# Performance work log

Hardware: AMD Instinct MI355X
Metric: run time of the kernel (lower is better)

Reference implementation:

```python
import jax, jax.numpy as jnp
import numpy as np

B, S, E, H, Dh = 2, 2048, 1024, 16, 64


def setup_inputs() -> dict:
    key = jax.random.key(0)
    ks = jax.random.split(key, 12)
    scale = 1.0 / np.sqrt(E)
    inp = {
        "query": jax.random.normal(ks[0], (B, S, E), jnp.float32),
        "key_": jax.random.normal(ks[1], (B, S, E), jnp.float32),
        "value": jax.random.normal(ks[2], (B, S, E), jnp.float32),
        # causal mask, broadcast over heads inside reference (mask==0 -> -inf)
        "mask": jnp.broadcast_to(jnp.tril(jnp.ones((S, S), jnp.int32)), (B, S, S)),
        "WQ": jax.random.normal(ks[3], (E, H * Dh), jnp.float32) * scale,
        "bQ": jnp.zeros((H * Dh,), jnp.float32),
        "WK": jax.random.normal(ks[4], (E, H * Dh), jnp.float32) * scale,
        "bK": jnp.zeros((H * Dh,), jnp.float32),
        "WV": jax.random.normal(ks[5], (E, H * Dh), jnp.float32) * scale,
        "bV": jnp.zeros((H * Dh,), jnp.float32),
        "WO": jax.random.normal(ks[6], (H * Dh, E), jnp.float32) * scale,
        "bO": jnp.zeros((E,), jnp.float32),
    }
    return inp


def reference(query, key_, value, mask, WQ, bQ, WK, bK, WV, bV, WO, bO):
    # projections -> [B, H, S, Dh]
    def proj(x, W, b):
        y = x @ W + b  # [B, S, H*Dh]
        return y.reshape(B, -1, H, Dh).transpose(0, 2, 1, 3)

    q = proj(query, WQ, bQ)
    k = proj(key_, WK, bK)
    v = proj(value, WV, bV)

    # scores [B, H, S, S]
    a = jnp.einsum("bhqd,bhkd->bhqk", q, k) / jnp.sqrt(jnp.float32(Dh))
    a = jnp.where(mask[:, None, :, :] == 0, -jnp.inf, a)
    alpha = jax.nn.softmax(a, axis=-1)
    z = jnp.einsum("bhqk,bhkd->bhqd", alpha, v)  # [B, H, S, Dh]
    z = z.transpose(0, 2, 1, 3).reshape(B, -1, H * Dh)
    return z @ WO + bO
```

## Files before the change

### kernel.cpp

```cpp
#include <hip/hip_runtime.h>
#include <hip/hip_bf16.h>
#include <math.h>

namespace {

constexpr int Bb = 2, Ss = 2048, Ee = 1024, Hh = 16, Dh = 64;
constexpr int M  = Bb * Ss;
constexpr int N  = Hh * Dh;
constexpr int Kd = Ee;

typedef __attribute__((ext_vector_type(8))) short bf16x8;
typedef __attribute__((ext_vector_type(4))) float f32x4;

__device__ inline unsigned short f2bf(float f) {
  return __builtin_bit_cast(unsigned short, __float2bfloat16(f));
}
__device__ inline unsigned pack2(float a, float b) {
  return (unsigned)f2bf(a) | ((unsigned)f2bf(b) << 16);
}
__device__ inline void load_lds16(const void* g, void* lds) {
  __builtin_amdgcn_global_load_lds((const __attribute__((address_space(1))) void*)g,
                                   (__attribute__((address_space(3))) void*)lds, 16, 0, 0);
}

__global__ __launch_bounds__(256) void convert3(const float* __restrict__ a0,
                                                const float* __restrict__ a1,
                                                const float* __restrict__ a2,
                                                unsigned short* __restrict__ o0,
                                                unsigned short* __restrict__ o1,
                                                unsigned short* __restrict__ o2) {
  const float* src = blockIdx.z == 0 ? a0 : (blockIdx.z == 1 ? a1 : a2);
  unsigned short* dst = blockIdx.z == 0 ? o0 : (blockIdx.z == 1 ? o1 : o2);
  size_t i = ((size_t)blockIdx.x * 256 + threadIdx.x) * 8;
  float4 u = ((const float4*)(src + i))[0];
  float4 v = ((const float4*)(src + i))[1];
  uint4 w;
  w.x = pack2(u.x, u.y);
  w.y = pack2(u.z, u.w);
  w.z = pack2(v.x, v.y);
  w.w = pack2(v.z, v.w);
  *((uint4*)(dst + i)) = w;
}

__global__ __launch_bounds__(256) void transposeW(const float* __restrict__ w0,
                                                  const float* __restrict__ w1,
                                                  const float* __restrict__ w2,
                                                  const float* __restrict__ w3,
                                                  unsigned short* __restrict__ t0,
                                                  unsigned short* __restrict__ t1,
                                                  unsigned short* __restrict__ t2,
                                                  unsigned short* __restrict__ t3) {
  const float* W = blockIdx.z == 0 ? w0 : (blockIdx.z == 1 ? w1 : (blockIdx.z == 2 ? w2 : w3));
  unsigned short* Wt = blockIdx.z == 0 ? t0 : (blockIdx.z == 1 ? t1 : (blockIdx.z == 2 ? t2 : t3));
  __shared__ float tl[32][33];
  const int t = threadIdx.x;
  const int r = t >> 5, c = t & 31;
  const int n0 = blockIdx.x * 32, k0 = blockIdx.y * 32;
#pragma unroll
  for (int i = 0; i < 4; ++i) tl[r + i * 8][c] = W[(size_t)(k0 + r + i * 8) * N + n0 + c];
  __syncthreads();
#pragma unroll
  for (int i = 0; i < 4; ++i) {
    int rr = r + i * 8;
    Wt[(size_t)(n0 + rr) * Kd + k0 + c] = f2bf(tl[c][rr]);
  }
}

__device__ __attribute__((always_inline)) inline void gemm_core(
    const unsigned short* __restrict__ A, const unsigned short* __restrict__ Wt,
    unsigned short* As0, unsigned short* As1, unsigned short* Bs0,
    unsigned short* Bs1, f32x4 (&acc)[4][4]) {
  const int t = threadIdx.x, l = t & 63, w = t >> 6;
  const int wr = w >> 1, wc = w & 1, lr = l & 15, kc = l >> 4;
  const int bm = blockIdx.y * 128, bn = blockIdx.x * 128;
  const int srow = t >> 2, sc4 = t & 3;
  const unsigned short* Ap1 = A + (size_t)(bm + srow) * Kd + sc4 * 8;
  const unsigned short* Ap2 = Ap1 + (size_t)64 * Kd;
  const unsigned short* Bp1 = Wt + (size_t)(bn + srow) * Kd + sc4 * 8;
  const unsigned short* Bp2 = Bp1 + (size_t)64 * Kd;
  const size_t d1 = (size_t)(w * 64) * 8, d2 = (size_t)(w * 64 + 256) * 8;

  auto stage = [&](unsigned short* Ab, unsigned short* Bb, int kk) {
    load_lds16(Ap1 + kk, Ab + d1);
    load_lds16(Ap2 + kk, Ab + d2);
    load_lds16(Bp1 + kk, Bb + d1);
    load_lds16(Bp2 + kk, Bb + d2);
  };
  auto compute = [&](const unsigned short* Ab, const unsigned short* Bb) {
    bf16x8 a[4], b[4];
#pragma unroll
    for (int m = 0; m < 4; ++m)
      a[m] = *(const bf16x8*)&Ab[(size_t)(wr * 64 + m * 16 + lr) * 32 + kc * 8];
#pragma unroll
    for (int n = 0; n < 4; ++n)
      b[n] = *(const bf16x8*)&Bb[(size_t)(wc * 64 + n * 16 + lr) * 32 + kc * 8];
#pragma unroll
    for (int m = 0; m < 4; ++m)
#pragma unroll
      for (int n = 0; n < 4; ++n)
        acc[m][n] = __builtin_amdgcn_mfma_f32_16x16x32_bf16(a[m], b[n], acc[m][n], 0, 0, 0);
  };

  stage(As0, Bs0, 0);
  __syncthreads();
  for (int kk = 0; kk < Kd; kk += 64) {
    if (kk + 32 < Kd) stage(As1, Bs1, kk + 32);
    compute(As0, Bs0);
    __syncthreads();
    if (kk + 64 < Kd) stage(As0, Bs0, kk + 64);
    compute(As1, Bs1);
    __syncthreads();
  }
}

__global__ __launch_bounds__(256) void qkv_gemm(
    const unsigned short* __restrict__ qb, const unsigned short* __restrict__ kb,
    const unsigned short* __restrict__ vb, const unsigned short* __restrict__ wqT,
    const unsigned short* __restrict__ wkT, const unsigned short* __restrict__ wvT,
    const float* __restrict__ bQ, const float* __restrict__ bK,
    const float* __restrict__ bV, unsigned short* __restrict__ Qw,
    unsigned short* __restrict__ Kw, unsigned short* __restrict__ Vt) {
  __shared__ alignas(16) unsigned short smem[4][128 * 32];
  const int z = blockIdx.z;
  const unsigned short* A  = z == 0 ? qb : (z == 1 ? kb : vb);
  const unsigned short* Wt = z == 0 ? wqT : (z == 1 ? wkT : wvT);
  const float* bias        = z == 0 ? bQ : (z == 1 ? bK : bV);

  f32x4 acc[4][4] = {};
  gemm_core(A, Wt, smem[0], smem[1], smem[2], smem[3], acc);

  const int t = threadIdx.x, l = t & 63, w = t >> 6;
  const int wr = w >> 1, wc = w & 1, lr = l & 15, kc = l >> 4;
  const int bm = blockIdx.y * 128, bn = blockIdx.x * 128;

  if (z <= 1) {
    unsigned short* Cout = z ? Kw : Qw;
    const float oscale = z ? 1.0f : 0.125f;
#pragma unroll
    for (int m = 0; m < 4; ++m)
#pragma unroll
      for (int n = 0; n < 4; ++n) {
        const int cg = bn + wc * 64 + n * 16 + lr;
        const float bv = bias[cg];
#pragma unroll
        for (int r = 0; r < 4; ++r) {
          const int rg = bm + wr * 64 + m * 16 + kc * 4 + r;
          const int b_ = rg >> 11, s = rg & (Ss - 1);
          const int h = cg >> 6, d = cg & 63;
          Cout[(((size_t)(b_ * Hh + h) * Ss + s) << 6) + d] =
              f2bf((acc[m][n][r] + bv) * oscale);
        }
      }
  } else {
    unsigned short(*Ct)[136] = reinterpret_cast<unsigned short(*)[136]>(&smem[0][0]);
    const int b_ = bm >> 11, sb = bm & (Ss - 1);
#pragma unroll
    for (int nh = 0; nh < 2; ++nh) {
      if (wc == nh) {
#pragma unroll
        for (int m = 0; m < 4; ++m)
#pragma unroll
          for (int n = 0; n < 4; ++n) {
            const int cg = bn + wc * 64 + n * 16 + lr;
            const float bv = bias[cg];
            const int cl = n * 16 + lr;
            const int s0 = wr * 64 + m * 16 + kc * 4;
            ushort4 pk;
            pk.x = f2bf(acc[m][n][0] + bv);
            pk.y = f2bf(acc[m][n][1] + bv);
            pk.z = f2bf(acc[m][n][2] + bv);
            pk.w = f2bf(acc[m][n][3] + bv);
            *(ushort4*)&Ct[cl][s0] = pk;
          }
      }
      __syncthreads();
#pragma unroll
      for (int i = 0; i < 4; ++i) {
        const int c = i * 256 + t;
        const int cl = c >> 4, ch = c & 15;
        const int cg = bn + nh * 64 + cl;
        const int h = cg >> 6, d = cg & 63;
        uint4 vv = *(const uint4*)&Ct[cl][ch * 8];
        *(uint4*)(Vt + (((size_t)(b_ * Hh + h) * Dh + d) << 11) + sb + ch * 8) = vv;
      }
      __syncthreads();
    }
  }
}

__global__ __launch_bounds__(256) void gemm_out(const unsigned short* __restrict__ A,
                                                const unsigned short* __restrict__ Wt,
                                                const float* __restrict__ bias,
                                                float* __restrict__ C) {
  __shared__ alignas(16) unsigned short smem[4][128 * 32];
  f32x4 acc[4][4] = {};
  gemm_core(A, Wt, smem[0], smem[1], smem[2], smem[3], acc);

  const int t = threadIdx.x, l = t & 63, w = t >> 6;
  const int wr = w >> 1, wc = w & 1, lr = l & 15, kc = l >> 4;
  const int bm = blockIdx.y * 128, bn = blockIdx.x * 128;
#pragma unroll
  for (int m = 0; m < 4; ++m)
#pragma unroll
    for (int n = 0; n < 4; ++n) {
      const int cg = bn + wc * 64 + n * 16 + lr;
      const float bv = bias[cg];
#pragma unroll
      for (int r = 0; r < 4; ++r) {
        const int rg = bm + wr * 64 + m * 16 + kc * 4 + r;
        C[(size_t)rg * N + cg] = acc[m][n][r] + bv;
      }
    }
}

__global__ __launch_bounds__(256) void attn_mfma(const unsigned short* __restrict__ Q,
                                                 const unsigned short* __restrict__ K,
                                                 const unsigned short* __restrict__ Vt,
                                                 unsigned short* __restrict__ Z) {
  __shared__ alignas(16) unsigned short Ks[64 * 64];
  __shared__ alignas(16) unsigned short Vs[64 * 64];
  __shared__ alignas(16) unsigned short Ps[4][16 * 64];

  const int bh  = blockIdx.x;
  const int qtA = blockIdx.y;
  const int qtB = (Ss / 64 - 1) - qtA;
  const int b  = bh >> 4, h = bh & 15;
  const int t  = threadIdx.x;
  const int l  = t & 63;
  const int w  = t >> 6;
  const int lr = l & 15;
  const int lg = l >> 4;

  const int qrowA = qtA * 64 + w * 16 + lr;
  const int qrowB = qtB * 64 + w * 16 + lr;
  const unsigned short* QpA = Q + ((size_t)bh * Ss + qrowA) * Dh;
  const unsigned short* QpB = Q + ((size_t)bh * Ss + qrowB) * Dh;
  bf16x8 bqA[2], bqB[2];
  bqA[0] = *(const bf16x8*)(QpA + lg * 8);
  bqA[1] = *(const bf16x8*)(QpA + 32 + lg * 8);
  bqB[0] = *(const bf16x8*)(QpB + lg * 8);
  bqB[1] = *(const bf16x8*)(QpB + 32 + lg * 8);

  f32x4 oA[4] = {}, oB[4] = {};
  float mA = -INFINITY, lA = 0.f, mB = -INFINITY, lB = 0.f;

  const int srow = l >> 3;
  const int scol = ((l & 7) ^ srow) * 16;
  const char* Kg = (const char*)(K + (size_t)bh * Ss * Dh);
  const char* Vg = (const char*)(Vt + (size_t)bh * Dh * Ss);
  unsigned short* kD0 = Ks + (w * 16) * 64;
  unsigned short* kD1 = Ks + (w * 16 + 8) * 64;
  unsigned short* vD0 = Vs + (w * 16) * 64;
  unsigned short* vD1 = Vs + (w * 16 + 8) * 64;
  const char* vr0 = Vg + (size_t)(w * 16 + srow) * (Ss * 2) + scol;
  const char* vr1 = Vg + (size_t)(w * 16 + 8 + srow) * (Ss * 2) + scol;

  const int rx = (lr & 7) << 4;

  auto process = [&](const bf16x8 (&bq)[2], f32x4 (&o)[4], float& mrow,
                     float& lsum, int qrow, bool diag, int kv0) {
    f32x4 sa[4];
    __builtin_amdgcn_s_setprio(1);
#pragma unroll
    for (int f = 0; f < 4; ++f) {
      sa[f] = (f32x4){0.f, 0.f, 0.f, 0.f};
#pragma unroll
      for (int kk = 0; kk < 2; ++kk) {
        const int cb = (kk * 64 + lg * 16) ^ rx;
        bf16x8 ak = *(const bf16x8*)((const char*)Ks + (f * 16 + lr) * 128 + cb);
        sa[f] = __builtin_amdgcn_mfma_f32_16x16x32_bf16(ak, bq[kk], sa[f], 0, 0, 0);
      }
    }
    __builtin_amdgcn_s_setprio(0);

    if (diag) {
#pragma unroll
      for (int f = 0; f < 4; ++f)
#pragma unroll
        for (int r = 0; r < 4; ++r) {
          const int kg = kv0 + f * 16 + lg * 4 + r;
          if (kg > qrow) sa[f][r] = -INFINITY;
        }
    }

    float pmax = sa[0][0];
#pragma unroll
    for (int f = 0; f < 4; ++f)
#pragma unroll
      for (int r = 0; r < 4; ++r) pmax = fmaxf(pmax, sa[f][r]);
    pmax = fmaxf(pmax, __shfl_xor(pmax, 16));
    pmax = fmaxf(pmax, __shfl_xor(pmax, 32));

    if (!__all(pmax <= mrow + 8.f)) {
      const float mnew = fmaxf(mrow, pmax);
      const float sc = __expf(mrow - mnew);
      lsum *= sc;
      float scr[4];
#pragma unroll
      for (int r = 0; r < 4; ++r) scr[r] = __shfl(sc, lg * 4 + r);
#pragma unroll
      for (int n = 0; n < 4; ++n)
#pragma unroll
        for (int r = 0; r < 4; ++r) o[n][r] *= scr[r];
      mrow = mnew;
    }

    float p[4][4];
    float psum = 0.f;
#pragma unroll
    for (int f = 0; f < 4; ++f)
#pragma unroll
      for (int r = 0; r < 4; ++r) {
        p[f][r] = __expf(sa[f][r] - mrow);
        psum += p[f][r];
      }
    psum += __shfl_xor(psum, 16);
    psum += __shfl_xor(psum, 32);
    lsum += psum;

    {
      char* Pw = (char*)Ps[w] + lr * 128;
#pragma unroll
      for (int f = 0; f < 4; ++f) {
        const int k0b = f * 32 + lg * 8;
        *(unsigned*)(Pw + ((k0b) ^ rx))     = pack2(p[f][0], p[f][1]);
        *(unsigned*)(Pw + ((k0b + 4) ^ rx)) = pack2(p[f][2], p[f][3]);
      }
    }

    __builtin_amdgcn_s_setprio(1);
#pragma unroll
    for (int kk = 0; kk < 2; ++kk) {
      const int cb = (kk * 64 + lg * 16) ^ rx;
      bf16x8 ap = *(const bf16x8*)((const char*)Ps[w] + lr * 128 + cb);
#pragma unroll
      for (int n = 0; n < 4; ++n) {
        bf16x8 bv = *(const bf16x8*)((const char*)Vs + (n * 16 + lr) * 128 + cb);
        o[n] = __builtin_amdgcn_mfma_f32_16x16x32_bf16(ap, bv, o[n], 0, 0, 0);
      }
    }
    __builtin_amdgcn_s_setprio(0);
  };

  for (int kt = 0; kt <= qtB; ++kt) {
    const int kv0 = kt * 64;
    __syncthreads();
    load_lds16(Kg + (size_t)(kv0 + w * 16 + srow) * 128 + scol, kD0);
    load_lds16(Kg + (size_t)(kv0 + w * 16 + 8 + srow) * 128 + scol, kD1);
    load_lds16(vr0 + kv0 * 2, vD0);
    load_lds16(vr1 + kv0 * 2, vD1);
    __syncthreads();

    process(bqB, oB, mB, lB, qrowB, kt == qtB, kv0);
    if (kt <= qtA) process(bqA, oA, mA, lA, qrowA, kt == qtA, kv0);
  }

  auto epilogue = [&](f32x4 (&o)[4], float lsum, int qt) {
    const float linv = 1.f / lsum;
    float li[4];
#pragma unroll
    for (int r = 0; r < 4; ++r) li[r] = __shfl(linv, lg * 4 + r);
#pragma unroll
    for (int n = 0; n < 4; ++n)
#pragma unroll
      for (int r = 0; r < 4; ++r) {
        const int qg = qt * 64 + w * 16 + lg * 4 + r;
        Z[((size_t)(b * Ss + qg)) * N + h * 64 + n * 16 + lr] =
            f2bf(o[n][r] * li[r]);
      }
  };
  epilogue(oA, lA, qtA);
  epilogue(oB, lB, qtB);
}

}

extern "C" void kernel_launch(void* const* d_in, const int* in_sizes, int n_in,
                              void* d_out, int out_size, void* d_ws, size_t ws_size,
                              hipStream_t stream) {
  const float* query = (const float*)d_in[0];
  const float* key_  = (const float*)d_in[1];
  const float* value = (const float*)d_in[2];
  const float* WQ = (const float*)d_in[4];
  const float* bQ = (const float*)d_in[5];
  const float* WK = (const float*)d_in[6];
  const float* bK = (const float*)d_in[7];
  const float* WV = (const float*)d_in[8];
  const float* bV = (const float*)d_in[9];
  const float* WO = (const float*)d_in[10];
  const float* bO = (const float*)d_in[11];
  float* out = (float*)d_out;

  const size_t mat = (size_t)M * N;
  unsigned short* qb  = (unsigned short*)d_ws;
  unsigned short* kb  = qb + mat;
  unsigned short* vb  = kb + mat;
  unsigned short* wqT = vb + mat;
  unsigned short* wkT = wqT + (size_t)N * Kd;
  unsigned short* wvT = wkT + (size_t)N * Kd;
  unsigned short* woT = wvT + (size_t)N * Kd;
  unsigned short* Qw  = woT + (size_t)N * Kd;
  unsigned short* Kw  = Qw + mat;
  unsigned short* Vw  = Kw + mat;
  unsigned short* zb  = qb;

  convert3<<<dim3(mat / 2048, 1, 3), 256, 0, stream>>>(query, key_, value, qb, kb, vb);
  transposeW<<<dim3(N / 32, Kd / 32, 4), 256, 0, stream>>>(WQ, WK, WV, WO, wqT, wkT, wvT, woT);

  qkv_gemm<<<dim3(N / 128, M / 128, 3), 256, 0, stream>>>(qb, kb, vb, wqT, wkT, wvT,
                                                          bQ, bK, bV, Qw, Kw, Vw);

  attn_mfma<<<dim3(Bb * Hh, Ss / 128), 256, 0, stream>>>(Qw, Kw, Vw, zb);

  gemm_out<<<dim3(N / 128, M / 128), 256, 0, stream>>>(zb, woT, bO, out);
}
```

Baseline: 255.3 us.

## Double-buffer K/V tiles in attention and deepen GEMM prefetch with vmcnt waits

The attention kernel now keeps two K/V tiles in LDS and prefetches tile kt+2 while computing on tile kt. The GEMM core keeps two stages in flight and replaces __syncthreads with explicit s_waitcnt vmcnt(4)/vmcnt(0) plus raw barriers. The goal is to hide global-to-LDS load latency behind MFMA work instead of stalling on it each iteration. In exchange the attention kernel doubles its LDS use for K/V, which may lower occupancy. Correctness depends on the hand-counted vmcnt values matching the number of outstanding loads per stage.

```diff
diff --git a/kernel.cpp b/kernel.cpp
--- a/kernel.cpp
+++ b/kernel.cpp
@@ -21,6 +21,18 @@
 __device__ inline void load_lds16(const void* g, void* lds) {
   __builtin_amdgcn_global_load_lds((const __attribute__((address_space(1))) void*)g,
                                    (__attribute__((address_space(3))) void*)lds, 16, 0, 0);
+}
+__device__ inline void wait_vm4_barrier() {
+  asm volatile("s_waitcnt vmcnt(4)" ::: "memory");
+  __builtin_amdgcn_s_barrier();
+}
+__device__ inline void wait_vm0_barrier() {
+  asm volatile("s_waitcnt vmcnt(0)" ::: "memory");
+  __builtin_amdgcn_s_barrier();
+}
+__device__ inline void barrier_then_fence() {
+  __builtin_amdgcn_s_barrier();
+  __builtin_amdgcn_sched_barrier(0);
 }
 
 __global__ __launch_bounds__(256) void convert3(const float* __restrict__ a0,
@@ -101,15 +113,20 @@
         acc[m][n] = __builtin_amdgcn_mfma_f32_16x16x32_bf16(a[m], b[n], acc[m][n], 0, 0, 0);
   };
 
+  constexpr int NT = Kd / 32;
   stage(As0, Bs0, 0);
-  __syncthreads();
-  for (int kk = 0; kk < Kd; kk += 64) {
-    if (kk + 32 < Kd) stage(As1, Bs1, kk + 32);
-    compute(As0, Bs0);
-    __syncthreads();
-    if (kk + 64 < Kd) stage(As0, Bs0, kk + 64);
-    compute(As1, Bs1);
-    __syncthreads();
+  stage(As1, Bs1, 32);
+#pragma unroll 2
+  for (int i = 0; i < NT; ++i) {
+    if (i + 1 < NT) wait_vm4_barrier();
+    else            wait_vm0_barrier();
+    if (i & 1) compute(As1, Bs1);
+    else       compute(As0, Bs0);
+    barrier_then_fence();
+    if (i + 2 < NT) {
+      if (i & 1) stage(As1, Bs1, (i + 2) * 32);
+      else       stage(As0, Bs0, (i + 2) * 32);
+    }
   }
 }
 
@@ -217,8 +234,8 @@
                                                  const unsigned short* __restrict__ K,
                                                  const unsigned short* __restrict__ Vt,
                                                  unsigned short* __restrict__ Z) {
-  __shared__ alignas(16) unsigned short Ks[64 * 64];
-  __shared__ alignas(16) unsigned short Vs[64 * 64];
+  __shared__ alignas(16) unsigned short Ks[2 * 64 * 64];
+  __shared__ alignas(16) unsigned short Vs[2 * 64 * 64];
   __shared__ alignas(16) unsigned short Ps[4][16 * 64];
 
   const int bh  = blockIdx.x;
@@ -248,17 +265,24 @@
   const int scol = ((l & 7) ^ srow) * 16;
   const char* Kg = (const char*)(K + (size_t)bh * Ss * Dh);
   const char* Vg = (const char*)(Vt + (size_t)bh * Dh * Ss);
-  unsigned short* kD0 = Ks + (w * 16) * 64;
-  unsigned short* kD1 = Ks + (w * 16 + 8) * 64;
-  unsigned short* vD0 = Vs + (w * 16) * 64;
-  unsigned short* vD1 = Vs + (w * 16 + 8) * 64;
   const char* vr0 = Vg + (size_t)(w * 16 + srow) * (Ss * 2) + scol;
   const char* vr1 = Vg + (size_t)(w * 16 + 8 + srow) * (Ss * 2) + scol;
 
   const int rx = (lr & 7) << 4;
 
+  auto stage_kv = [&](int kt) {
+    unsigned short* kb_ = Ks + (kt & 1) * 4096;
+    unsigned short* vb_ = Vs + (kt & 1) * 4096;
+    const size_t kv0 = (size_t)kt * 64;
+    load_lds16(Kg + (kv0 + w * 16 + srow) * 128 + scol, kb_ + (w * 16) * 64);
+    load_lds16(Kg + (kv0 + w * 16 + 8 + srow) * 128 + scol, kb_ + (w * 16 + 8) * 64);
+    load_lds16(vr0 + kv0 * 2, vb_ + (w * 16) * 64);
+    load_lds16(vr1 + kv0 * 2, vb_ + (w * 16 + 8) * 64);
+  };
+
   auto process = [&](const bf16x8 (&bq)[2], f32x4 (&o)[4], float& mrow,
-                     float& lsum, int qrow, bool diag, int kv0) {
+                     float& lsum, int qrow, bool diag, int kv0,
+                     const unsigned short* Ksb, const unsigned short* Vsb) {
     f32x4 sa[4];
     __builtin_amdgcn_s_setprio(1);
 #pragma unroll
@@ -267,7 +291,7 @@
 #pragma unroll
       for (int kk = 0; kk < 2; ++kk) {
         const int cb = (kk * 64 + lg * 16) ^ rx;
-        bf16x8 ak = *(const bf16x8*)((const char*)Ks + (f * 16 + lr) * 128 + cb);
+        bf16x8 ak = *(const bf16x8*)((const char*)Ksb + (f * 16 + lr) * 128 + cb);
         sa[f] = __builtin_amdgcn_mfma_f32_16x16x32_bf16(ak, bq[kk], sa[f], 0, 0, 0);
       }
     }
@@ -335,24 +359,25 @@
       bf16x8 ap = *(const bf16x8*)((const char*)Ps[w] + lr * 128 + cb);
 #pragma unroll
       for (int n = 0; n < 4; ++n) {
-        bf16x8 bv = *(const bf16x8*)((const char*)Vs + (n * 16 + lr) * 128 + cb);
+        bf16x8 bv = *(const bf16x8*)((const char*)Vsb + (n * 16 + lr) * 128 + cb);
         o[n] = __builtin_amdgcn_mfma_f32_16x16x32_bf16(ap, bv, o[n], 0, 0, 0);
       }
     }
     __builtin_amdgcn_s_setprio(0);
   };
 
+  stage_kv(0);
+  stage_kv(1);
   for (int kt = 0; kt <= qtB; ++kt) {
+    if (kt < qtB) wait_vm4_barrier();
+    else          wait_vm0_barrier();
+    const unsigned short* kb_ = Ks + (kt & 1) * 4096;
+    const unsigned short* vb_ = Vs + (kt & 1) * 4096;
     const int kv0 = kt * 64;
-    __syncthreads();
-    load_lds16(Kg + (size_t)(kv0 + w * 16 + srow) * 128 + scol, kD0);
-    load_lds16(Kg + (size_t)(kv0 + w * 16 + 8 + srow) * 128 + scol, kD1);
-    load_lds16(vr0 + kv0 * 2, vD0);
-    load_lds16(vr1 + kv0 * 2, vD1);
-    __syncthreads();
-
-    process(bqB, oB, mB, lB, qrowB, kt == qtB, kv0);
-    if (kt <= qtA) process(bqA, oA, mA, lA, qrowA, kt == qtA, kv0);
+    process(bqB, oB, mB, lB, qrowB, kt == qtB, kv0, kb_, vb_);
+    if (kt <= qtA) process(bqA, oA, mA, lA, qrowA, kt == qtA, kv0, kb_, vb_);
+    barrier_then_fence();
+    if (kt + 2 <= qtB) stage_kv(kt + 2);
   }
 
   auto epilogue = [&](f32x4 (&o)[4], float lsum, int qt) {
```

Measured after the change: 246.7 us. -3.4%, faster.
